# Kernel optimization log

Measured on AMD Instinct MI355X. Metric: run time of the kernel, lower is better.

The kernel has to match this reference:

```python
import jax, jax.numpy as jnp
import numpy as np


def _chamfer(src, tgt):
    # src: [B, N, 3], tgt: [B, M, 3]
    x2 = jnp.sum(src * src, axis=-1)              # [B, N]
    y2 = jnp.sum(tgt * tgt, axis=-1)              # [B, M]
    xy = jnp.einsum('bnd,bmd->bnm', src, tgt)     # [B, N, M]
    d2 = x2[:, :, None] + y2[:, None, :] - 2.0 * xy
    d2 = jnp.maximum(d2, 0.0)                     # guard tiny negatives
    cham_x = jnp.min(d2, axis=2)                  # [B, N] min over tgt
    cham_y = jnp.min(d2, axis=1)                  # [B, M] min over src
    # point_reduction='mean', batch_reduction='sum'
    loss = jnp.sum(jnp.mean(cham_x, axis=1)) + jnp.sum(jnp.mean(cham_y, axis=1))
    return loss


def setup_inputs() -> dict:
    key = jax.random.key(0)
    k1, k2 = jax.random.split(key)
    src = jax.random.normal(k1, (16, 4096, 3), dtype=jnp.float32)
    tgt = jax.random.normal(k2, (16, 4096, 3), dtype=jnp.float32)
    return {"src": src, "tgt": tgt}


def reference(src, tgt):
    wgeo = 1.0
    return wgeo * _chamfer(src, tgt)
```

## Files before the change

### kernel.cpp

```cpp
#include <hip/hip_runtime.h>
#include <hip/hip_bf16.h>


#define BATCH   16
#define NPTS    4096
#define NSTRIPS 32
#define CHUNKC  512
#define NCHUNKS (NPTS / CHUNKC)
#define NSTEP   (CHUNKC / 64)

typedef __attribute__((ext_vector_type(8)))  short short8;
typedef __attribute__((ext_vector_type(16))) float float16;

union U4S8 { uint4 u; short8 s; };

__device__ inline unsigned int bfb(float v) {
    __hip_bfloat16 h = __float2bfloat16(v);
    unsigned short u; __builtin_memcpy(&u, &h, 2);
    return (unsigned int)u;
}
__device__ inline float bff(float v) { return __bfloat162float(__float2bfloat16(v)); }

#define ONEB 0x3F80u

__device__ inline void buildA(float x, float y, float z, uint4& w0, uint4& w1) {
    float xhf = bff(x), yhf = bff(y), zhf = bff(z);
    float f = fmaf(x, x, fmaf(y, y, z * z));
    float fhf = bff(f);
    unsigned xh = bfb(xhf), yh = bfb(yhf), zh = bfb(zhf);
    unsigned xl = bfb(x - xhf), yl = bfb(y - yhf), zl = bfb(z - zhf);
    unsigned fh = bfb(fhf), fl = bfb(f - fhf);
    w0 = make_uint4(xh | (yh << 16), zh | (xh << 16),
                    yh | (zh << 16), xl | (yl << 16));
    w1 = make_uint4(zl | (fh << 16), fl | (ONEB << 16), ONEB, 0u);
}

__device__ inline void buildB(float x, float y, float z, uint4& w0, uint4& w1) {
    float xhf = bff(x), yhf = bff(y), zhf = bff(z);
    float f = fmaf(x, x, fmaf(y, y, z * z));
    float fhf = bff(f);
    unsigned a = bfb(-2.0f * xhf), b = bfb(-2.0f * yhf), c = bfb(-2.0f * zhf);
    unsigned d = bfb(-2.0f * (x - xhf)), e = bfb(-2.0f * (y - yhf)),
             g = bfb(-2.0f * (z - zhf));
    unsigned fh = bfb(fhf), fl = bfb(f - fhf);
    w0 = make_uint4(a | (b << 16), c | (d << 16),
                    e | (g << 16), a | (b << 16));
    w1 = make_uint4(c | (ONEB << 16), ONEB | (fh << 16), fl, 0u);
}

__device__ inline float tree16(const float16& a) {
    float m0 = fminf(fminf(a[0],  a[1]),  a[2]);
    float m1 = fminf(fminf(a[3],  a[4]),  a[5]);
    float m2 = fminf(fminf(a[6],  a[7]),  a[8]);
    float m3 = fminf(fminf(a[9],  a[10]), a[11]);
    float m4 = fminf(fminf(a[12], a[13]), a[14]);
    float p0 = fminf(fminf(m0, m1), a[15]);
    float p1 = fminf(fminf(m2, m3), m4);
    return fminf(p0, p1);
}

__global__ __launch_bounds__(256, 3) void chamfer_main(
    const float* __restrict__ src, const float* __restrict__ tgt,
    unsigned* __restrict__ wsC, float* __restrict__ out)
{
    __shared__ uint4 sbuf[2][2][CHUNKC];
    __shared__ unsigned colpart[NPTS];
    __shared__ float wsum[4];

    int blk = blockIdx.x;
    const int strip = blk & (NSTRIPS - 1);
    const int b     = blk >> 5;

    const int t    = threadIdx.x;
    const int lane = t & 63;
    const int w    = t >> 6;
    const int h    = lane >> 5;
    const int l5   = lane & 31;

    const float* Araw = src + (size_t)b * NPTS * 3;
    const float* Braw = tgt + (size_t)b * NPTS * 3;

    short8 afr;
    {
        int row = strip * 128 + w * 32 + l5;
        uint4 w0, w1;
        buildA(Araw[3 * row], Araw[3 * row + 1], Araw[3 * row + 2], w0, w1);
        U4S8 tt; tt.u = h ? w1 : w0;
        afr = tt.s;
    }

#pragma unroll
    for (int i = 0; i < 16; i++) colpart[t + i * 256] = 0xFFFFFFFFu;

    float nx[2][3];
    auto loadRaw = [&](int c) {
#pragma unroll
        for (int k = 0; k < 2; k++) {
            int p = c * CHUNKC + t + k * 256;
            nx[k][0] = Braw[3 * p + 0];
            nx[k][1] = Braw[3 * p + 1];
            nx[k][2] = Braw[3 * p + 2];
        }
    };
    auto convertWrite = [&](int bi) {
#pragma unroll
        for (int k = 0; k < 2; k++) {
            int lp = t + k * 256;
            uint4 w0, w1;
            buildB(nx[k][0], nx[k][1], nx[k][2], w0, w1);
            sbuf[bi][0][lp] = w0;
            sbuf[bi][1][lp] = w1;
        }
    };

    const float16 z16 = {0.f,0.f,0.f,0.f,0.f,0.f,0.f,0.f,
                         0.f,0.f,0.f,0.f,0.f,0.f,0.f,0.f};
    float rm[16];
#pragma unroll
    for (int r = 0; r < 16; r++) rm[r] = 1e30f;

    loadRaw(0);
    convertWrite(0);
    for (int c = 0; c < NCHUNKS; c++) {
        __syncthreads();
        if (c + 1 < NCHUNKS) loadRaw(c + 1);
        const int bi = c & 1;

        U4S8 c0, c1, n0, n1;
        c0.u = sbuf[bi][h][l5];
        c1.u = sbuf[bi][h][32 + l5];
#pragma unroll 4
        for (int j2 = 0; j2 < NSTEP; j2++) {
            int nj = (j2 + 1) & (NSTEP - 1);
            n0.u = sbuf[bi][h][nj * 64 + l5];
            n1.u = sbuf[bi][h][nj * 64 + 32 + l5];
            float16 a0 = __builtin_amdgcn_mfma_f32_32x32x16_bf16(afr, c0.s, z16, 0, 0, 0);
            float16 a1 = __builtin_amdgcn_mfma_f32_32x32x16_bf16(afr, c1.s, z16, 0, 0, 0);
#pragma unroll
            for (int r = 0; r < 16; r++)
                rm[r] = fminf(fminf(a0[r], a1[r]), rm[r]);
            float cm0 = tree16(a0);
            float cm1 = tree16(a1);
            const int col = c * CHUNKC + j2 * 64 + l5;
            atomicMin(&colpart[col],      __float_as_uint(fmaxf(cm0, 0.0f)));
            atomicMin(&colpart[col + 32], __float_as_uint(fmaxf(cm1, 0.0f)));
            c0 = n0; c1 = n1;
        }
        if (c + 1 < NCHUNKS) convertWrite((c + 1) & 1);
    }

    __syncthreads();
#pragma unroll
    for (int i = 0; i < 16; i++) {
        const int idx = t + i * 256;
        atomicMin(&wsC[(size_t)b * NPTS + idx], colpart[idx]);
    }

#pragma unroll
    for (int mask = 1; mask <= 16; mask <<= 1)
#pragma unroll
        for (int r = 0; r < 16; r++)
            rm[r] = fminf(rm[r], __shfl_xor(rm[r], mask, 64));

    float s = 0.0f;
#pragma unroll
    for (int r = 0; r < 16; r++) s += fmaxf(rm[r], 0.0f);
    s += __shfl_xor(s, 32, 64);

    if (lane == 0) wsum[w] = s;
    __syncthreads();
    if (t == 0)
        atomicAdd(out, (wsum[0] + wsum[1] + wsum[2] + wsum[3]) * (1.0f / (float)NPTS));
}

__global__ __launch_bounds__(256) void finish_reduce(
    const unsigned* __restrict__ wsC, float* __restrict__ out)
{
    __shared__ float wsum[4];
    const int b = blockIdx.x;
    float v = 0.0f;
#pragma unroll
    for (int i = 0; i < 16; i++)
        v += __uint_as_float(wsC[(size_t)b * NPTS + threadIdx.x + i * 256]);
#pragma unroll
    for (int mask = 1; mask <= 32; mask <<= 1) v += __shfl_xor(v, mask, 64);
    if ((threadIdx.x & 63) == 0) wsum[threadIdx.x >> 6] = v;
    __syncthreads();
    if (threadIdx.x == 0)
        atomicAdd(out, (wsum[0] + wsum[1] + wsum[2] + wsum[3]) * (1.0f / (float)NPTS));
}

extern "C" void kernel_launch(void* const* d_in, const int* in_sizes, int n_in,
                              void* d_out, int out_size, void* d_ws, size_t ws_size,
                              hipStream_t stream)
{
    const float* src = (const float*)d_in[0];
    const float* tgt = (const float*)d_in[1];
    float* out = (float*)d_out;
    unsigned* wsC = (unsigned*)d_ws;

    hipMemsetAsync(out, 0, sizeof(float), stream);
    hipMemsetAsync(wsC, 0xFF, (size_t)BATCH * NPTS * sizeof(unsigned), stream);
    chamfer_main <<<BATCH * NSTRIPS, 256, 0, stream>>>(src, tgt, wsC, out);
    finish_reduce<<<BATCH, 256, 0, stream>>>(wsC, out);
}
```

Baseline: 82.50 us.

## Split target columns across two blocks per strip and reduce row minima globally

Each block now handles only half of the target points, which doubles the grid to 1024 blocks and halves the shared-memory column buffer. Row minima are therefore partial, so they go through LDS and a global atomicMin into a second workspace, and the finish kernel sums both workspaces. The launch-bounds occupancy hint rises from 3 to 4 blocks per CU. The goal is better CU fill and latency hiding; the cost is redundant A-fragment builds, extra global atomics and a larger memset.

```diff
diff --git a/kernel.cpp b/kernel.cpp
--- a/kernel.cpp
+++ b/kernel.cpp
@@ -5,8 +5,10 @@
 #define BATCH   16
 #define NPTS    4096
 #define NSTRIPS 32
+#define NH      2
+#define COLS_PB 2048
 #define CHUNKC  512
-#define NCHUNKS (NPTS / CHUNKC)
+#define NCHUNKS (COLS_PB / CHUNKC)
 #define NSTEP   (CHUNKC / 64)
 
 typedef __attribute__((ext_vector_type(8)))  short short8;
@@ -59,17 +61,18 @@
     return fminf(p0, p1);
 }
 
-__global__ __launch_bounds__(256, 3) void chamfer_main(
+__global__ __launch_bounds__(256, 4) void chamfer_main(
     const float* __restrict__ src, const float* __restrict__ tgt,
-    unsigned* __restrict__ wsC, float* __restrict__ out)
+    unsigned* __restrict__ wsC, unsigned* __restrict__ wsR)
 {
     __shared__ uint4 sbuf[2][2][CHUNKC];
-    __shared__ unsigned colpart[NPTS];
-    __shared__ float wsum[4];
+    __shared__ unsigned colpart[COLS_PB];
 
     int blk = blockIdx.x;
-    const int strip = blk & (NSTRIPS - 1);
-    const int b     = blk >> 5;
+    const int strip = blk & (NSTRIPS - 1); blk >>= 5;
+    const int b     = blk & 15;            blk >>= 4;
+    const int q     = blk;
+    const int qoff  = q * COLS_PB;
 
     const int t    = threadIdx.x;
     const int lane = t & 63;
@@ -90,13 +93,13 @@
     }
 
 #pragma unroll
-    for (int i = 0; i < 16; i++) colpart[t + i * 256] = 0xFFFFFFFFu;
+    for (int i = 0; i < COLS_PB / 256; i++) colpart[t + i * 256] = 0xFFFFFFFFu;
 
     float nx[2][3];
     auto loadRaw = [&](int c) {
 #pragma unroll
         for (int k = 0; k < 2; k++) {
-            int p = c * CHUNKC + t + k * 256;
+            int p = qoff + c * CHUNKC + t + k * 256;
             nx[k][0] = Braw[3 * p + 0];
             nx[k][1] = Braw[3 * p + 1];
             nx[k][2] = Braw[3 * p + 2];
@@ -151,9 +154,9 @@
 
     __syncthreads();
 #pragma unroll
-    for (int i = 0; i < 16; i++) {
+    for (int i = 0; i < COLS_PB / 256; i++) {
         const int idx = t + i * 256;
-        atomicMin(&wsC[(size_t)b * NPTS + idx], colpart[idx]);
+        atomicMin(&wsC[(size_t)b * NPTS + qoff + idx], colpart[idx]);
     }
 
 #pragma unroll
@@ -162,19 +165,22 @@
         for (int r = 0; r < 16; r++)
             rm[r] = fminf(rm[r], __shfl_xor(rm[r], mask, 64));
 
-    float s = 0.0f;
-#pragma unroll
-    for (int r = 0; r < 16; r++) s += fmaxf(rm[r], 0.0f);
-    s += __shfl_xor(s, 32, 64);
-
-    if (lane == 0) wsum[w] = s;
-    __syncthreads();
-    if (t == 0)
-        atomicAdd(out, (wsum[0] + wsum[1] + wsum[2] + wsum[3]) * (1.0f / (float)NPTS));
+    __syncthreads();
+    if (l5 == 0) {
+#pragma unroll
+        for (int r = 0; r < 16; r++) {
+            const int row = w * 32 + (r & 3) + 8 * (r >> 2) + 4 * h;
+            colpart[row] = __float_as_uint(fmaxf(rm[r], 0.0f));
+        }
+    }
+    __syncthreads();
+    if (t < 128)
+        atomicMin(&wsR[(size_t)b * NPTS + strip * 128 + t], colpart[t]);
 }
 
 __global__ __launch_bounds__(256) void finish_reduce(
-    const unsigned* __restrict__ wsC, float* __restrict__ out)
+    const unsigned* __restrict__ wsC, const unsigned* __restrict__ wsR,
+    float* __restrict__ out)
 {
     __shared__ float wsum[4];
     const int b = blockIdx.x;
@@ -182,6 +188,9 @@
 #pragma unroll
     for (int i = 0; i < 16; i++)
         v += __uint_as_float(wsC[(size_t)b * NPTS + threadIdx.x + i * 256]);
+#pragma unroll
+    for (int i = 0; i < 16; i++)
+        v += __uint_as_float(wsR[(size_t)b * NPTS + threadIdx.x + i * 256]);
 #pragma unroll
     for (int mask = 1; mask <= 32; mask <<= 1) v += __shfl_xor(v, mask, 64);
     if ((threadIdx.x & 63) == 0) wsum[threadIdx.x >> 6] = v;
@@ -198,9 +207,10 @@
     const float* tgt = (const float*)d_in[1];
     float* out = (float*)d_out;
     unsigned* wsC = (unsigned*)d_ws;
+    unsigned* wsR = wsC + (size_t)BATCH * NPTS;
 
     hipMemsetAsync(out, 0, sizeof(float), stream);
-    hipMemsetAsync(wsC, 0xFF, (size_t)BATCH * NPTS * sizeof(unsigned), stream);
-    chamfer_main <<<BATCH * NSTRIPS, 256, 0, stream>>>(src, tgt, wsC, out);
-    finish_reduce<<<BATCH, 256, 0, stream>>>(wsC, out);
-}
+    hipMemsetAsync(d_ws, 0xFF, (size_t)2 * BATCH * NPTS * sizeof(unsigned), stream);
+    chamfer_main <<<NH * BATCH * NSTRIPS, 256, 0, stream>>>(src, tgt, wsC, wsR);
+    finish_reduce<<<BATCH, 256, 0, stream>>>(wsC, wsR, out);
+}
```

New measurement: 78.67 us. -4.6%, faster.
